# Kernel optimization log

Hardware: AMD Instinct MI355X
Metric: run time of the kernel (lower is better)

The kernel has to match this reference:

```python
import jax, jax.numpy as jnp
import numpy as np

N_NODES = 100000


def setup_inputs() -> dict:
    key = jax.random.key(0)
    k1, k2, k3, k4 = jax.random.split(key, 4)
    E = 1600000
    in_dim, out_dim = 256, 64
    h = jax.random.normal(k1, (N_NODES, in_dim), dtype=jnp.float32)
    src = jax.random.randint(k2, (E,), 0, N_NODES, dtype=jnp.int64)
    dst = jax.random.randint(k3, (E,), 0, N_NODES, dtype=jnp.int64)
    W = jax.random.normal(k4, (in_dim, out_dim), dtype=jnp.float32) * (1.0 / np.sqrt(in_dim))
    b = jnp.zeros((out_dim,), dtype=jnp.float32)
    return {"h": h, "src": src, "dst": dst, "W": W, "b": b}


def reference(h, src, dst, W, b):
    # dgl GraphConv, norm='both': out = D_in^{-1/2} A D_out^{-1/2} h W + b
    E = src.shape[0]
    ones = jnp.ones((E,), dtype=h.dtype)
    deg_out = jax.ops.segment_sum(ones, src, num_segments=N_NODES)  # out-degree of src nodes
    deg_in = jax.ops.segment_sum(ones, dst, num_segments=N_NODES)   # in-degree of dst nodes
    norm_src = jnp.clip(deg_out, 1.0, None) ** -0.5                  # [N]
    norm_dst = jnp.clip(deg_in, 1.0, None) ** -0.5                   # [N]
    # in_dim > out_dim: project first (as dgl does), then aggregate small features
    x = (h * norm_src[:, None]) @ W                                  # [N, out_dim]
    msgs = x[src]                                                    # [E, out_dim] gather
    agg = jax.ops.segment_sum(msgs, dst, num_segments=N_NODES)      # [N, out_dim] scatter-add
    out = agg * norm_dst[:, None] + b
    # ReLU; dropout is identity in eval mode
    return jax.nn.relu(out)
```

## Files before the change

### kernel.cpp

```cpp
#include <hip/hip_runtime.h>
#include <hip/hip_fp16.h>

#define N_NODES 100000
#define IN_DIM 256
#define OUT_DIM 64
#define NT 782
#define NSC 512
#define SMAX 3200
#define CAP_F 3072

typedef _Float16 half8 __attribute__((ext_vector_type(8)));
typedef float f32x4 __attribute__((ext_vector_type(4)));

__global__ __launch_bounds__(256) void init_kernel(int* __restrict__ cursor,
                                                   int* __restrict__ deg_out) {
    int i = blockIdx.x * 256 + threadIdx.x;
    if (i < N_NODES) deg_out[i] = 0;
    if (i < NT) cursor[i] = 0;
}

__global__ __launch_bounds__(256) void scatter_kernel(const int* __restrict__ src,
                                                      const int* __restrict__ dst,
                                                      int* __restrict__ cursor,
                                                      int* __restrict__ binnedD,
                                                      int* __restrict__ deg_out,
                                                      int E, int chunk) {
    __shared__ int sorted[SMAX];
    __shared__ unsigned short sbin[SMAX];
    __shared__ int hist[NT];
    __shared__ int boff[NT + 1];
    __shared__ int resv[NT];
    const int t = threadIdx.x, blk = blockIdx.x;
    const int lo = blk * chunk;
    int hiA = lo + chunk; if (hiA > E) hiA = E;
    for (int s0 = lo; s0 < hiA; s0 += SMAX) {
        int m = hiA - s0; if (m > SMAX) m = SMAX;
        for (int i = t; i < NT; i += 256) hist[i] = 0;
        __syncthreads();
        for (int k = t; k < m; k += 256) {
            int s = src[s0 + k], d = dst[s0 + k];
            atomicAdd(&deg_out[s], 1);
            atomicAdd(&hist[d >> 7], 1);
        }
        __syncthreads();
        if (t < 64) {
            int carry = 0;
            for (int r = 0; r < (NT + 63) / 64; ++r) {
                int i = r * 64 + t;
                int v = (i < NT) ? hist[i] : 0;
                int incl = v;
#pragma unroll
                for (int off = 1; off < 64; off <<= 1) {
                    int y = __shfl_up(incl, off);
                    if (t >= off) incl += y;
                }
                if (i < NT) boff[i] = carry + incl - v;
                carry += __shfl(incl, 63);
            }
            if (t == 0) boff[NT] = carry;
        }
        __syncthreads();
        for (int i = t; i < NT; i += 256) {
            int h = hist[i];
            if (h) resv[i] = atomicAdd(&cursor[i], h);
            hist[i] = boff[i];
        }
        __syncthreads();
        for (int k = t; k < m; k += 256) {
            int s = src[s0 + k], d = dst[s0 + k];
            int bin = d >> 7;
            int p = atomicAdd(&hist[bin], 1);
            sorted[p] = (s << 7) | (d & 127);
            sbin[p] = (unsigned short)bin;
        }
        __syncthreads();
        for (int k = t; k < m; k += 256) {
            int b = sbin[k];
            int loc = resv[b] + (k - boff[b]);
            if (loc < CAP_F) binnedD[b * CAP_F + loc] = sorted[k];
        }
        __syncthreads();
    }
}

__global__ __launch_bounds__(256) void tile_kernel(const int* __restrict__ cursor,
                                                   const int* __restrict__ binnedD,
                                                   int* __restrict__ csr,
                                                   int* __restrict__ offs, int* __restrict__ cnt) {
    __shared__ int h[128], cur[128];
    __shared__ int w0tot;
    const int bin = blockIdx.x, t = threadIdx.x, lane = t & 63;
    if (t < 128) h[t] = 0;
    __syncthreads();

    const int base = bin * CAP_F;
    int m = cursor[bin]; if (m > CAP_F) m = CAP_F;
    for (int k = t; k < m; k += 256) atomicAdd(&h[binnedD[base + k] & 127], 1);
    __syncthreads();
    int v = (t < 128) ? h[t] : 0;
    int incl = v;
#pragma unroll
    for (int off = 1; off < 64; off <<= 1) {
        int y = __shfl_up(incl, off);
        if (lane >= off) incl += y;
    }
    if (t == 63) w0tot = incl;
    __syncthreads();
    int excl = incl - v + ((t >= 64 && t < 128) ? w0tot : 0);
    if (t < 128) {
        cur[t] = excl;
        int node = bin * 128 + t;
        if (node < N_NODES) { offs[node] = base + excl; cnt[node] = v; }
    }
    __syncthreads();
    for (int k = t; k < m; k += 256) {
        int rec = binnedD[base + k];
        int p = atomicAdd(&cur[rec & 127], 1);
        csr[base + p] = rec >> 7;
    }
}

#define A_LD 136
__global__ __launch_bounds__(256) void gemm_kernel(const float* __restrict__ hmat,
                                                   const float* __restrict__ W,
                                                   const int* __restrict__ deg_out,
                                                   __half* __restrict__ xh) {
    __shared__ _Float16 sA[64 * A_LD];
    __shared__ _Float16 sB[64 * A_LD];
    const int t = threadIdx.x;
    const int lane = t & 63;
    const int w = t >> 6;
    const int row0 = blockIdx.x * 64;
    const int m0 = (w & 1) * 32;
    const int n0 = (w >> 1) * 32;

    f32x4 acc00 = {0.f, 0.f, 0.f, 0.f}, acc01 = {0.f, 0.f, 0.f, 0.f};
    f32x4 acc10 = {0.f, 0.f, 0.f, 0.f}, acc11 = {0.f, 0.f, 0.f, 0.f};

    for (int khalf = 0; khalf < 2; ++khalf) {
        const int k0 = khalf * 128;
        __syncthreads();
#pragma unroll
        for (int it = 0; it < 8; ++it) {
            int f = t + it * 256;
            int row = f >> 5;
            int c4 = f & 31;
            int grow = row0 + row; if (grow >= N_NODES) grow = N_NODES - 1;
            float4 v = *(const float4*)(hmat + (size_t)grow * IN_DIM + k0 + c4 * 4);
            _Float16 p[4];
            p[0] = (_Float16)v.x; p[1] = (_Float16)v.y;
            p[2] = (_Float16)v.z; p[3] = (_Float16)v.w;
            *(uint2*)&sA[row * A_LD + c4 * 4] = *(uint2*)p;
        }
        {
            int n = t & 63;
            int kk0 = (t >> 6) * 32;
#pragma unroll
            for (int kb = 0; kb < 8; ++kb) {
                _Float16 p[4];
#pragma unroll
                for (int u = 0; u < 4; ++u)
                    p[u] = (_Float16)W[(size_t)(k0 + kk0 + kb * 4 + u) * OUT_DIM + n];
                *(uint2*)&sB[n * A_LD + kk0 + kb * 4] = *(uint2*)p;
            }
        }
        __syncthreads();
#pragma unroll
        for (int kb = 0; kb < 4; ++kb) {
            int koff = kb * 32 + (lane >> 4) * 8;
            half8 a0 = *(const half8*)&sA[(m0 + (lane & 15)) * A_LD + koff];
            half8 a1 = *(const half8*)&sA[(m0 + 16 + (lane & 15)) * A_LD + koff];
            half8 b0 = *(const half8*)&sB[(n0 + (lane & 15)) * A_LD + koff];
            half8 b1 = *(const half8*)&sB[(n0 + 16 + (lane & 15)) * A_LD + koff];
            acc00 = __builtin_amdgcn_mfma_f32_16x16x32_f16(a0, b0, acc00, 0, 0, 0);
            acc01 = __builtin_amdgcn_mfma_f32_16x16x32_f16(a0, b1, acc01, 0, 0, 0);
            acc10 = __builtin_amdgcn_mfma_f32_16x16x32_f16(a1, b0, acc10, 0, 0, 0);
            acc11 = __builtin_amdgcn_mfma_f32_16x16x32_f16(a1, b1, acc11, 0, 0, 0);
        }
    }

    const int col16 = lane & 15;
    const int rq = (lane >> 4) * 4;
#pragma unroll
    for (int mi = 0; mi < 2; ++mi) {
        float nrm[4];
#pragma unroll
        for (int r = 0; r < 4; ++r) {
            int row = row0 + m0 + mi * 16 + rq + r;
            int d = (row < N_NODES) ? deg_out[row] : 1;
            nrm[r] = rsqrtf((float)(d < 1 ? 1 : d));
        }
#pragma unroll
        for (int ni = 0; ni < 2; ++ni) {
            const f32x4 a = (mi == 0) ? (ni == 0 ? acc00 : acc01)
                                      : (ni == 0 ? acc10 : acc11);
            int col = n0 + ni * 16 + col16;
#pragma unroll
            for (int r = 0; r < 4; ++r) {
                int row = row0 + m0 + mi * 16 + rq + r;
                if (row < N_NODES)
                    xh[(size_t)row * OUT_DIM + col] = __float2half(a[r] * nrm[r]);
            }
        }
    }
}

__global__ __launch_bounds__(256) void aggregate_kernel(const int* __restrict__ offs,
                                                        const int* __restrict__ cnt,
                                                        const int* __restrict__ csr,
                                                        const __half* __restrict__ xh,
                                                        const float* __restrict__ b,
                                                        float* __restrict__ out) {
    const int t = threadIdx.x;
    const int lane = t & 63;
    const int wid = t >> 6;
    const int node = blockIdx.x * 4 + wid;
    const int g = lane >> 3;
    const int c = lane & 7;

    const int start = offs[node];
    const int n = cnt[node];

    float acc[8] = {0.f, 0.f, 0.f, 0.f, 0.f, 0.f, 0.f, 0.f};
    for (int base = 0; base < n; base += 64) {
        int k = base + lane;
        int sidx = (k < n) ? csr[start + k] : 0;
        int m = n - base; if (m > 64) m = 64;
        for (int e0 = 0; e0 < m; e0 += 16) {
            int ea = e0 + g;
            int eb = e0 + 8 + g;
            int sa = __shfl(sidx, ea);
            int sb = __shfl(sidx, eb);
            bool va = ea < m;
            bool vb = eb < m;
            float wa = va ? 1.f : 0.f;
            float wb = vb ? 1.f : 0.f;
            uint4 ra = *(const uint4*)(xh + (size_t)(va ? sa : 0) * OUT_DIM + 8 * c);
            const bool grpb = (e0 + 8) < m;
            uint4 rb;
            if (grpb)
                rb = *(const uint4*)(xh + (size_t)(vb ? sb : 0) * OUT_DIM + 8 * c);
            {
                const __half2* hp = (const __half2*)&ra;
#pragma unroll
                for (int p = 0; p < 4; ++p) {
                    float2 f = __half22float2(hp[p]);
                    acc[2 * p]     = fmaf(wa, f.x, acc[2 * p]);
                    acc[2 * p + 1] = fmaf(wa, f.y, acc[2 * p + 1]);
                }
            }
            if (grpb) {
                const __half2* hp = (const __half2*)&rb;
#pragma unroll
                for (int p = 0; p < 4; ++p) {
                    float2 f = __half22float2(hp[p]);
                    acc[2 * p]     = fmaf(wb, f.x, acc[2 * p]);
                    acc[2 * p + 1] = fmaf(wb, f.y, acc[2 * p + 1]);
                }
            }
        }
    }

#pragma unroll
    for (int off = 8; off < 64; off <<= 1) {
#pragma unroll
        for (int p = 0; p < 8; ++p)
            acc[p] += __shfl_xor(acc[p], off);
    }

    if (g == 0) {
        float nrm = rsqrtf((float)(n < 1 ? 1 : n));
        float4 bv0 = *(const float4*)&b[c * 8];
        float4 bv1 = *(const float4*)&b[c * 8 + 4];
        float4 r0, r1;
        r0.x = fmaxf(fmaf(acc[0], nrm, bv0.x), 0.f);
        r0.y = fmaxf(fmaf(acc[1], nrm, bv0.y), 0.f);
        r0.z = fmaxf(fmaf(acc[2], nrm, bv0.z), 0.f);
        r0.w = fmaxf(fmaf(acc[3], nrm, bv0.w), 0.f);
        r1.x = fmaxf(fmaf(acc[4], nrm, bv1.x), 0.f);
        r1.y = fmaxf(fmaf(acc[5], nrm, bv1.y), 0.f);
        r1.z = fmaxf(fmaf(acc[6], nrm, bv1.z), 0.f);
        r1.w = fmaxf(fmaf(acc[7], nrm, bv1.w), 0.f);
        float4* orow = (float4*)(out + (size_t)node * OUT_DIM + c * 8);
        orow[0] = r0;
        orow[1] = r1;
    }
}

extern "C" void kernel_launch(void* const* d_in, const int* in_sizes, int n_in,
                              void* d_out, int out_size, void* d_ws, size_t ws_size,
                              hipStream_t stream) {
    const float* h   = (const float*)d_in[0];
    const int*   src = (const int*)d_in[1];
    const int*   dst = (const int*)d_in[2];
    const float* W   = (const float*)d_in[3];
    const float* b   = (const float*)d_in[4];
    float* out = (float*)d_out;
    const int E = in_sizes[1];
    const int chunkS = (E + NSC - 1) / NSC;

    char* ws = (char*)d_ws;
    int*    cursor  = (int*)(ws);
    int*    deg_out = (int*)(ws + 3328);
    int*    binnedD = (int*)(ws + 403328);
    int*    csr     = (int*)(ws + 10012544);
    int*    offs    = (int*)(ws + 19621760);
    int*    cntA    = (int*)(ws + 20021760);
    __half* xh      = (__half*)(ws + 20421760);

    init_kernel<<<(N_NODES + 255) / 256, 256, 0, stream>>>(cursor, deg_out);
    scatter_kernel<<<NSC, 256, 0, stream>>>(src, dst, cursor, binnedD, deg_out, E, chunkS);
    tile_kernel<<<NT, 256, 0, stream>>>(cursor, binnedD, csr, offs, cntA);
    gemm_kernel<<<(N_NODES + 63) / 64, 256, 0, stream>>>(h, W, deg_out, xh);
    aggregate_kernel<<<N_NODES / 4, 256, 0, stream>>>(offs, cntA, csr, xh, b, out);
}
```

Baseline: 306.1 us.

## Replace global deg_out atomics with source-binned byte counting and in-place CSR

Out-degree is no longer counted with 1.6M random global atomics. Each edge's low source byte is binned by source tile into a byte buffer, and tile_kernel counts each tile's degrees with shared-memory atomics. The CSR is staged in shared memory and written back over binnedD, which shrinks the workspace and removes the large zero-init of deg_out. The cost is a second histogram, scan and scatter pass in scatter_kernel, plus more shared memory that may lower occupancy.

```diff
diff --git a/kernel.cpp b/kernel.cpp
--- a/kernel.cpp
+++ b/kernel.cpp
@@ -12,89 +12,105 @@
 typedef _Float16 half8 __attribute__((ext_vector_type(8)));
 typedef float f32x4 __attribute__((ext_vector_type(4)));
 
-__global__ __launch_bounds__(256) void init_kernel(int* __restrict__ cursor,
-                                                   int* __restrict__ deg_out) {
-    int i = blockIdx.x * 256 + threadIdx.x;
-    if (i < N_NODES) deg_out[i] = 0;
-    if (i < NT) cursor[i] = 0;
+__global__ __launch_bounds__(256) void init_kernel(int* __restrict__ cursorD,
+                                                   int* __restrict__ cursorS) {
+    for (int i = threadIdx.x; i < NT; i += 256) { cursorD[i] = 0; cursorS[i] = 0; }
 }
 
 __global__ __launch_bounds__(256) void scatter_kernel(const int* __restrict__ src,
                                                       const int* __restrict__ dst,
-                                                      int* __restrict__ cursor,
+                                                      int* __restrict__ cursorD,
+                                                      int* __restrict__ cursorS,
                                                       int* __restrict__ binnedD,
-                                                      int* __restrict__ deg_out,
+                                                      unsigned char* __restrict__ srcb,
                                                       int E, int chunk) {
     __shared__ int sorted[SMAX];
     __shared__ unsigned short sbin[SMAX];
-    __shared__ int hist[NT];
-    __shared__ int boff[NT + 1];
-    __shared__ int resv[NT];
+    __shared__ unsigned char sortedB[SMAX];
+    __shared__ unsigned short sbinS[SMAX];
+    __shared__ int histD[NT], boffD[NT], resvD[NT];
+    __shared__ int histS[NT], boffS[NT], resvS[NT];
     const int t = threadIdx.x, blk = blockIdx.x;
+    const int lane = t & 63, wv = t >> 6;
     const int lo = blk * chunk;
     int hiA = lo + chunk; if (hiA > E) hiA = E;
     for (int s0 = lo; s0 < hiA; s0 += SMAX) {
         int m = hiA - s0; if (m > SMAX) m = SMAX;
-        for (int i = t; i < NT; i += 256) hist[i] = 0;
+        for (int i = t; i < NT; i += 256) { histD[i] = 0; histS[i] = 0; }
         __syncthreads();
         for (int k = t; k < m; k += 256) {
             int s = src[s0 + k], d = dst[s0 + k];
-            atomicAdd(&deg_out[s], 1);
-            atomicAdd(&hist[d >> 7], 1);
-        }
-        __syncthreads();
-        if (t < 64) {
+            atomicAdd(&histD[d >> 7], 1);
+            atomicAdd(&histS[s >> 7], 1);
+        }
+        __syncthreads();
+        if (wv < 2) {
+            int* hsrc = (wv == 0) ? histD : histS;
+            int* bdst = (wv == 0) ? boffD : boffS;
             int carry = 0;
             for (int r = 0; r < (NT + 63) / 64; ++r) {
-                int i = r * 64 + t;
-                int v = (i < NT) ? hist[i] : 0;
+                int i = r * 64 + lane;
+                int v = (i < NT) ? hsrc[i] : 0;
                 int incl = v;
 #pragma unroll
                 for (int off = 1; off < 64; off <<= 1) {
                     int y = __shfl_up(incl, off);
-                    if (t >= off) incl += y;
+                    if (lane >= off) incl += y;
                 }
-                if (i < NT) boff[i] = carry + incl - v;
+                if (i < NT) bdst[i] = carry + incl - v;
                 carry += __shfl(incl, 63);
             }
-            if (t == 0) boff[NT] = carry;
         }
         __syncthreads();
         for (int i = t; i < NT; i += 256) {
-            int h = hist[i];
-            if (h) resv[i] = atomicAdd(&cursor[i], h);
-            hist[i] = boff[i];
+            int hd = histD[i];
+            if (hd) resvD[i] = atomicAdd(&cursorD[i], hd);
+            int hs = histS[i];
+            if (hs) resvS[i] = atomicAdd(&cursorS[i], hs);
+            histD[i] = boffD[i];
+            histS[i] = boffS[i];
         }
         __syncthreads();
         for (int k = t; k < m; k += 256) {
             int s = src[s0 + k], d = dst[s0 + k];
-            int bin = d >> 7;
-            int p = atomicAdd(&hist[bin], 1);
+            int bd = d >> 7;
+            int p = atomicAdd(&histD[bd], 1);
             sorted[p] = (s << 7) | (d & 127);
-            sbin[p] = (unsigned short)bin;
+            sbin[p] = (unsigned short)bd;
+            int bs = s >> 7;
+            int ps = atomicAdd(&histS[bs], 1);
+            sortedB[ps] = (unsigned char)(s & 127);
+            sbinS[ps] = (unsigned short)bs;
         }
         __syncthreads();
         for (int k = t; k < m; k += 256) {
             int b = sbin[k];
-            int loc = resv[b] + (k - boff[b]);
+            int loc = resvD[b] + (k - boffD[b]);
             if (loc < CAP_F) binnedD[b * CAP_F + loc] = sorted[k];
-        }
-        __syncthreads();
-    }
-}
-
-__global__ __launch_bounds__(256) void tile_kernel(const int* __restrict__ cursor,
+            int bs = sbinS[k];
+            int locS = resvS[bs] + (k - boffS[bs]);
+            if (locS < CAP_F) srcb[bs * CAP_F + locS] = sortedB[k];
+        }
+        __syncthreads();
+    }
+}
+
+__global__ __launch_bounds__(256) void tile_kernel(const int* __restrict__ cursorD,
+                                                   const int* __restrict__ cursorS,
                                                    const int* __restrict__ binnedD,
+                                                   const unsigned char* __restrict__ srcb,
                                                    int* __restrict__ csr,
-                                                   int* __restrict__ offs, int* __restrict__ cnt) {
+                                                   int* __restrict__ offs, int* __restrict__ cnt,
+                                                   int* __restrict__ deg_out) {
     __shared__ int h[128], cur[128];
+    __shared__ int lcsr[CAP_F];
     __shared__ int w0tot;
     const int bin = blockIdx.x, t = threadIdx.x, lane = t & 63;
     if (t < 128) h[t] = 0;
     __syncthreads();
 
     const int base = bin * CAP_F;
-    int m = cursor[bin]; if (m > CAP_F) m = CAP_F;
+    int m = cursorD[bin]; if (m > CAP_F) m = CAP_F;
     for (int k = t; k < m; k += 256) atomicAdd(&h[binnedD[base + k] & 127], 1);
     __syncthreads();
     int v = (t < 128) ? h[t] : 0;
@@ -116,7 +132,21 @@
     for (int k = t; k < m; k += 256) {
         int rec = binnedD[base + k];
         int p = atomicAdd(&cur[rec & 127], 1);
-        csr[base + p] = rec >> 7;
+        lcsr[p] = rec >> 7;
+    }
+    __syncthreads();
+    for (int k = t; k < m; k += 256) csr[base + k] = lcsr[k];
+
+    __syncthreads();
+    if (t < 128) h[t] = 0;
+    __syncthreads();
+    int ms = cursorS[bin]; if (ms > CAP_F) ms = CAP_F;
+    const int sbase = bin * CAP_F;
+    for (int k = t; k < ms; k += 256) atomicAdd(&h[srcb[sbase + k]], 1);
+    __syncthreads();
+    if (t < 128) {
+        int node = bin * 128 + t;
+        if (node < N_NODES) deg_out[node] = h[t];
     }
 }
 
@@ -300,17 +330,19 @@
     const int chunkS = (E + NSC - 1) / NSC;
 
     char* ws = (char*)d_ws;
-    int*    cursor  = (int*)(ws);
-    int*    deg_out = (int*)(ws + 3328);
-    int*    binnedD = (int*)(ws + 403328);
-    int*    csr     = (int*)(ws + 10012544);
-    int*    offs    = (int*)(ws + 19621760);
-    int*    cntA    = (int*)(ws + 20021760);
-    __half* xh      = (__half*)(ws + 20421760);
-
-    init_kernel<<<(N_NODES + 255) / 256, 256, 0, stream>>>(cursor, deg_out);
-    scatter_kernel<<<NSC, 256, 0, stream>>>(src, dst, cursor, binnedD, deg_out, E, chunkS);
-    tile_kernel<<<NT, 256, 0, stream>>>(cursor, binnedD, csr, offs, cntA);
+    int*           cursorD = (int*)(ws);
+    int*           cursorS = (int*)(ws + 3328);
+    int*           binnedD = (int*)(ws + 6656);
+    int*           csr     = binnedD;
+    unsigned char* srcb    = (unsigned char*)(ws + 9615872);
+    int*           offs    = (int*)(ws + 12018176);
+    int*           cntA    = (int*)(ws + 12418176);
+    int*           deg_out = (int*)(ws + 12818176);
+    __half*        xh      = (__half*)(ws + 13218176);
+
+    init_kernel<<<1, 256, 0, stream>>>(cursorD, cursorS);
+    scatter_kernel<<<NSC, 256, 0, stream>>>(src, dst, cursorD, cursorS, binnedD, srcb, E, chunkS);
+    tile_kernel<<<NT, 256, 0, stream>>>(cursorD, cursorS, binnedD, srcb, csr, offs, cntA, deg_out);
     gemm_kernel<<<(N_NODES + 63) / 64, 256, 0, stream>>>(h, W, deg_out, xh);
     aggregate_kernel<<<N_NODES / 4, 256, 0, stream>>>(offs, cntA, csr, xh, b, out);
 }
```

Measured after the change: 263.5 us. 13.9% less time.
